# Kernel optimization log

Hardware: AMD Instinct MI355X
Metric: run time of the kernel (lower is better)

The kernel has to match this reference:

```python
import jax, jax.numpy as jnp
import numpy as np

H, W = 512, 512          # config.height, config.width
PIXEL_SIZE = 1.0
A2P = 1.0 / PIXEL_SIZE   # angstrom_to_pixel
INV_AREA = 1.0 / PIXEL_SIZE ** 2
SQRT2 = 1.4142135623730951
N, F, B = 8192, 2, 8


def setup_inputs() -> dict:
    key = jax.random.key(0)
    k1, k2, k3, k4, k5 = jax.random.split(key, 5)
    centers = jax.random.uniform(k1, (N, 3), minval=64.0, maxval=448.0)
    scales = jax.random.uniform(k2, (N, F), minval=1.0, maxval=4.0)
    weights = jax.random.normal(k3, (N, F))
    bubble_weights = 0.1 * jax.random.normal(k4, (N,))
    transform_matrix = jnp.eye(4)[None] + 0.01 * jax.random.normal(k5, (B, 4, 4))
    return {
        "transform_matrix": transform_matrix,
        "centers": centers,
        "scales": scales,
        "weights": weights,
        "bubble_weights": bubble_weights,
    }


def _pixel_profile(c, s, n):
    # Exact integral of a 1D gaussian N(c, s^2) over each unit pixel [x-0.5, x+0.5].
    # c, s: (M,) -> (M, n)
    x = jnp.arange(n, dtype=c.dtype)
    lo = (x[None, :] - 0.5 - c[:, None]) / (s[:, None] * SQRT2)
    hi = (x[None, :] + 0.5 - c[:, None]) / (s[:, None] * SQRT2)
    return 0.5 * (jax.lax.erf(hi) - jax.lax.erf(lo))


def _splat_point_masses(img, cp, w):
    # Bilinear scatter-add of point masses at projected centers cp (N,2), coord0 = row.
    r, c = cp[:, 0], cp[:, 1]
    r0f, c0f = jnp.floor(r), jnp.floor(c)
    fr, fc = r - r0f, c - c0f
    r0, c0 = r0f.astype(jnp.int32), c0f.astype(jnp.int32)
    for dr, dc, ww in ((0, 0, (1 - fr) * (1 - fc)), (0, 1, (1 - fr) * fc),
                       (1, 0, fr * (1 - fc)), (1, 1, fr * fc)):
        rr = jnp.clip(r0 + dr, 0, H - 1)
        cc = jnp.clip(c0 + dc, 0, W - 1)
        img = img.at[rr, cc].add(w * ww)
    return img


def _render_one(cp, scales_px_flat, weights_flat, bubble_weights):
    # cp: (N, 2) projected centers in pixel units.
    cpe = jnp.repeat(cp, F, axis=0)                       # (N*F, 2): expand per scale
    ph = _pixel_profile(cpe[:, 0], scales_px_flat, H)     # (N*F, H)
    pw = _pixel_profile(cpe[:, 1], scales_px_flat, W)     # (N*F, W)
    img = jnp.einsum("mh,mw->hw", weights_flat[:, None] * ph, pw)
    img = _splat_point_masses(img, cp, bubble_weights)
    return img


def reference(transform_matrix, centers, scales, weights, bubble_weights):
    # Homogenize centers: (N, 4)
    ch = jnp.concatenate([centers, jnp.ones_like(centers[:, :1])], axis=-1)
    # Solve T x = c for each (pose, gaussian): (B,1,4,4) \\ (1,N,4,1) -> (B,N,4)
    proj = jnp.linalg.solve(transform_matrix[:, None], ch[None, :, :, None])[..., 0]
    cp = proj[..., :2] / proj[..., 3:4] * A2P             # (B, N, 2) pixel coords
    scales_px = (scales * A2P).reshape(-1)                # (N*F,)
    weights_flat = weights.reshape(-1)                    # (N*F,)
    render = jax.vmap(lambda c: _render_one(c, scales_px, weights_flat, bubble_weights))
    result = render(cp) * INV_AREA                        # (B, H, W)
    return result
```

## Files before the change

### kernel.cpp

```cpp
#include <hip/hip_runtime.h>
#include <hip/hip_bf16.h>

#define HH 512
#define WW 512
#define NN 8192
#define FF 2
#define BB 8
#define MM (NN * FF)
#define HW (HH * WW)
#define NC (BB * NN)

#define NSIG 3.8f

__device__ __forceinline__ float ld(const void* p, int i, int f32mode) {
  if (f32mode) return ((const float*)p)[i];
  unsigned u = ((const unsigned short*)p)[i];
  return __uint_as_float(u << 16);
}

__device__ __forceinline__ float readlane_f(float v, int l) {
  return __uint_as_float(__builtin_amdgcn_readlane(__float_as_uint(v), l));
}

__device__ __forceinline__ float erf_f(float x) {
  float ax = fabsf(x);
  float t = 1.0f / (1.0f + 0.3275911f * ax);
  float y = t * (0.254829592f +
           t * (-0.284496736f +
           t * (1.421413741f +
           t * (-1.453152027f +
           t * 1.061405429f))));
  y = 1.0f - y * __expf(-ax * ax);
  return copysignf(y, x);
}

__global__ void k_inv(const void* __restrict__ T, float* __restrict__ invT,
                      int* __restrict__ flag) {
  int b = threadIdx.x;
  if (b >= BB) return;
  const float* Tf = (const float*)T;
  int f32mode = (fabsf(Tf[0] - 1.f) < 0.4f &&
                 fabsf(Tf[5] - 1.f) < 0.4f &&
                 fabsf(Tf[10] - 1.f) < 0.4f) ? 1 : 0;
  if (b == 0) *flag = f32mode;

  float a[4][8];
  for (int r = 0; r < 4; ++r)
    for (int c = 0; c < 4; ++c) {
      a[r][c] = ld(T, b * 16 + r * 4 + c, f32mode);
      a[r][4 + c] = (r == c) ? 1.0f : 0.0f;
    }
  for (int k = 0; k < 4; ++k) {
    int p = k; float best = fabsf(a[k][k]);
    for (int i = k + 1; i < 4; ++i) {
      float v = fabsf(a[i][k]);
      if (v > best) { best = v; p = i; }
    }
    if (p != k)
      for (int c = 0; c < 8; ++c) { float tmp = a[k][c]; a[k][c] = a[p][c]; a[p][c] = tmp; }
    float inv = 1.0f / a[k][k];
    for (int c = 0; c < 8; ++c) a[k][c] *= inv;
    for (int i = 0; i < 4; ++i) {
      if (i == k) continue;
      float f = a[i][k];
      for (int c = 0; c < 8; ++c) a[i][c] -= f * a[k][c];
    }
  }
  for (int r = 0; r < 4; ++r)
    for (int c = 0; c < 4; ++c)
      invT[b * 16 + r * 4 + c] = a[r][4 + c];
}

__global__ void k_table(const void* __restrict__ centers, const void* __restrict__ scales,
                        const void* __restrict__ weights, const void* __restrict__ bubble,
                        const float* __restrict__ invT, const int* __restrict__ flag,
                        float4* __restrict__ tabA, float4* __restrict__ tabB,
                        float4* __restrict__ img4) {
  int idx = blockIdx.x * blockDim.x + threadIdx.x;
  int stride = gridDim.x * blockDim.x;
  for (int j = idx; j < BB * HW / 4; j += stride)
    img4[j] = make_float4(0.f, 0.f, 0.f, 0.f);
  if (idx >= NC) return;
  int f32mode = *flag;
  int b = idx >> 13;
  int n = idx & (NN - 1);
  const float* Tb = invT + b * 16;
  float cx = ld(centers, 3 * n, f32mode);
  float cy = ld(centers, 3 * n + 1, f32mode);
  float cz = ld(centers, 3 * n + 2, f32mode);
  float p0 = Tb[0]  * cx + Tb[1]  * cy + Tb[2]  * cz + Tb[3];
  float p1 = Tb[4]  * cx + Tb[5]  * cy + Tb[6]  * cz + Tb[7];
  float p3 = Tb[12] * cx + Tb[13] * cy + Tb[14] * cz + Tb[15];
  float inv = 1.0f / p3;
  float4 A, Bv;
  A.x = p0 * inv;
  A.y = p1 * inv;
  A.z = ld(scales, 2 * n, f32mode);
  A.w = ld(weights, 2 * n, f32mode);
  Bv.x = ld(scales, 2 * n + 1, f32mode);
  Bv.y = ld(weights, 2 * n + 1, f32mode);
  Bv.z = ld(bubble, n, f32mode);
  Bv.w = 0.f;
  tabA[idx] = A;
  tabB[idx] = Bv;
}

__global__ void k_splat(const float4* __restrict__ tabA, const float4* __restrict__ tabB,
                        float* __restrict__ img) {
  int gid = blockIdx.x * blockDim.x + threadIdx.x;
  int lane = gid & 63;
  int nwaves = (gridDim.x * blockDim.x) >> 6;
  int wave = __builtin_amdgcn_readfirstlane(gid >> 6);

  int i = wave;
  float4 A = make_float4(0.f, 0.f, 1.f, 0.f);
  float4 Bv = make_float4(1.f, 0.f, 0.f, 0.f);
  if (i < NC) { A = tabA[i]; Bv = tabB[i]; }

  while (i < NC) {
    int in = i + nwaves;
    float4 An = A, Bn = Bv;
    if (in < NC) { An = tabA[in]; Bn = tabB[in]; }

    float row = A.x, col = A.y, s0 = A.z, w0 = A.w;
    float s1 = Bv.x, w1 = Bv.y, bw = Bv.z;
    float* imgb = img + ((size_t)(i >> 13) << 18);

    {
      float r0f = floorf(row), c0f = floorf(col);
      float fr = row - r0f, fc = col - c0f;
      int r0 = (int)r0f, c0 = (int)c0f;
      int rr0 = min(max(r0, 0), HH - 1), rr1 = min(max(r0 + 1, 0), HH - 1);
      int cc0 = min(max(c0, 0), WW - 1), cc1 = min(max(c0 + 1, 0), WW - 1);
      int rsel = (lane < 2) ? rr0 : rr1;
      int csel = (lane & 1) ? cc1 : cc0;
      float wr = (lane < 2) ? (1.f - fr) : fr;
      float wc = (lane & 1) ? fc : (1.f - fc);
      if (lane < 4)
        unsafeAtomicAdd(imgb + (rsel << 9) + csel, bw * wr * wc);
    }

    float smax = fmaxf(s0, s1);
    float rs0 = 0.70710678118f / s0;
    float rs1 = 0.70710678118f / s1;
    float Rf = NSIG * smax + 0.5f;
    int rlo = max(0, (int)ceilf(row - Rf));
    int rhi = min(HH - 1, (int)floorf(row + Rf));
    int clo = max(0, (int)ceilf(col - Rf));
    int chi = min(WW - 1, (int)floorf(col + Rf));
    if (rlo <= rhi && clo <= chi) {
      int nc = chi - clo + 1;
      int nr = rhi - rlo + 1;
      float xc = (float)(clo + lane) - 0.5f - col;
      float x0 = xc * rs0;
      float pw0 = (erf_f(x0 + rs0) - erf_f(x0)) * (0.25f * w0);
      float x1 = xc * rs1;
      float pw1 = (erf_f(x1 + rs1) - erf_f(x1)) * (0.25f * w1);
      float yr = (float)(rlo + lane) - 0.5f - row;
      float y0 = yr * rs0;
      float Dh0 = erf_f(y0 + rs0) - erf_f(y0);
      float y1 = yr * rs1;
      float Dh1 = erf_f(y1 + rs1) - erf_f(y1);
      float* base = imgb + (rlo << 9) + clo + lane;
      for (int k = 0; k < nr; ++k) {
        float val = readlane_f(Dh0, k) * pw0 + readlane_f(Dh1, k) * pw1;
        if (lane < nc)
          unsafeAtomicAdd(base + (k << 9), val);
      }
    }

    i = in; A = An; Bv = Bn;
  }
}

__global__ void k_final(const float4* __restrict__ img4, const int* __restrict__ flag,
                        void* __restrict__ out) {
  int idx = blockIdx.x * blockDim.x + threadIdx.x;
  int stride = gridDim.x * blockDim.x;
  int f32mode = *flag;
  if (f32mode) {
    float4* o = (float4*)out;
    for (int j = idx; j < BB * HW / 4; j += stride)
      o[j] = img4[j];
  } else {
    ushort4* o = (ushort4*)out;
    for (int j = idx; j < BB * HW / 4; j += stride) {
      float4 v = img4[j];
      __hip_bfloat16 h0 = __float2bfloat16(v.x);
      __hip_bfloat16 h1 = __float2bfloat16(v.y);
      __hip_bfloat16 h2 = __float2bfloat16(v.z);
      __hip_bfloat16 h3 = __float2bfloat16(v.w);
      ushort4 t;
      t.x = *reinterpret_cast<unsigned short*>(&h0);
      t.y = *reinterpret_cast<unsigned short*>(&h1);
      t.z = *reinterpret_cast<unsigned short*>(&h2);
      t.w = *reinterpret_cast<unsigned short*>(&h3);
      o[j] = t;
    }
  }
}

extern "C" void kernel_launch(void* const* d_in, const int* in_sizes, int n_in,
                              void* d_out, int out_size, void* d_ws, size_t ws_size,
                              hipStream_t stream) {
  const void* T       = d_in[0];
  const void* centers = d_in[1];
  const void* scales  = d_in[2];
  const void* weights = d_in[3];
  const void* bubble  = d_in[4];

  char* ws = (char*)d_ws;
  size_t off = 0;
  float*  img  = (float*)(ws + off);  off += (size_t)BB * HW * 4;
  float4* tabA = (float4*)(ws + off); off += (size_t)NC * 16;
  float4* tabB = (float4*)(ws + off); off += (size_t)NC * 16;
  float*  invT = (float*)(ws + off);  off += (size_t)BB * 16 * 4;
  int*    flag = (int*)(ws + off);

  k_inv<<<1, 64, 0, stream>>>(T, invT, flag);
  k_table<<<512, 256, 0, stream>>>(centers, scales, weights, bubble, invT, flag,
                                   tabA, tabB, (float4*)img);
  k_splat<<<2048, 256, 0, stream>>>(tabA, tabB, img);
  k_final<<<512, 256, 0, stream>>>((const float4*)img, flag, d_out);
}
```

Measured before the change: 540.9 us.

## Bin gaussians by image and row band before splatting for atomic locality

Adds a counting-sort pass (per-block bin counts, a scan, and a scatter fill) that reorders the per-gaussian table by image index and 64-row band. The splat kernel then reads the image index from the table instead of deriving it from position. The intent is to make concurrently running waves hit nearby image regions, improving cache locality of the atomic adds. This costs two extra small launches, a serial scan, and possibly more atomic contention on shared addresses.

```diff
diff --git a/kernel.cpp b/kernel.cpp
--- a/kernel.cpp
+++ b/kernel.cpp
@@ -11,6 +11,9 @@
 #define NC (BB * NN)
 
 #define NSIG 3.8f
+
+#define NBINS 64
+#define CBLK 256
 
 __device__ __forceinline__ float ld(const void* p, int i, int f32mode) {
   if (f32mode) return ((const float*)p)[i];
@@ -34,6 +37,26 @@
   return copysignf(y, x);
 }
 
+__device__ __forceinline__ void project(const void* centers, const float* invT,
+                                        int b, int n, int f32mode,
+                                        float& row, float& col) {
+  const float* Tb = invT + b * 16;
+  float cx = ld(centers, 3 * n, f32mode);
+  float cy = ld(centers, 3 * n + 1, f32mode);
+  float cz = ld(centers, 3 * n + 2, f32mode);
+  float p0 = Tb[0]  * cx + Tb[1]  * cy + Tb[2]  * cz + Tb[3];
+  float p1 = Tb[4]  * cx + Tb[5]  * cy + Tb[6]  * cz + Tb[7];
+  float p3 = Tb[12] * cx + Tb[13] * cy + Tb[14] * cz + Tb[15];
+  float inv = 1.0f / p3;
+  row = p0 * inv;
+  col = p1 * inv;
+}
+
+__device__ __forceinline__ int bin_of(float row, int b) {
+  int band = min(max((int)row, 0), HH - 1) >> 6;
+  return (b << 3) | band;
+}
+
 __global__ void k_inv(const void* __restrict__ T, float* __restrict__ invT,
                       int* __restrict__ flag) {
   int b = threadIdx.x;
@@ -71,38 +94,72 @@
       invT[b * 16 + r * 4 + c] = a[r][4 + c];
 }
 
-__global__ void k_table(const void* __restrict__ centers, const void* __restrict__ scales,
-                        const void* __restrict__ weights, const void* __restrict__ bubble,
-                        const float* __restrict__ invT, const int* __restrict__ flag,
-                        float4* __restrict__ tabA, float4* __restrict__ tabB,
-                        float4* __restrict__ img4) {
-  int idx = blockIdx.x * blockDim.x + threadIdx.x;
-  int stride = gridDim.x * blockDim.x;
-  for (int j = idx; j < BB * HW / 4; j += stride)
+__global__ void __launch_bounds__(CBLK)
+k_cnt(const void* __restrict__ centers, const float* __restrict__ invT,
+      const int* __restrict__ flag, int* __restrict__ blkcnt,
+      float4* __restrict__ img4) {
+  __shared__ int cnt[NBINS];
+  int tid = threadIdx.x;
+  if (tid < NBINS) cnt[tid] = 0;
+  __syncthreads();
+  int idx = blockIdx.x * CBLK + tid;
+  for (int j = idx; j < BB * HW / 4; j += NC)
     img4[j] = make_float4(0.f, 0.f, 0.f, 0.f);
-  if (idx >= NC) return;
   int f32mode = *flag;
-  int b = idx >> 13;
-  int n = idx & (NN - 1);
-  const float* Tb = invT + b * 16;
-  float cx = ld(centers, 3 * n, f32mode);
-  float cy = ld(centers, 3 * n + 1, f32mode);
-  float cz = ld(centers, 3 * n + 2, f32mode);
-  float p0 = Tb[0]  * cx + Tb[1]  * cy + Tb[2]  * cz + Tb[3];
-  float p1 = Tb[4]  * cx + Tb[5]  * cy + Tb[6]  * cz + Tb[7];
-  float p3 = Tb[12] * cx + Tb[13] * cy + Tb[14] * cz + Tb[15];
-  float inv = 1.0f / p3;
+  int b = idx >> 13, n = idx & (NN - 1);
+  float row, col;
+  project(centers, invT, b, n, f32mode, row, col);
+  atomicAdd(&cnt[bin_of(row, b)], 1);
+  __syncthreads();
+  if (tid < NBINS) blkcnt[blockIdx.x * NBINS + tid] = cnt[tid];
+}
+
+__global__ void k_scan(int* __restrict__ blkcnt) {
+  __shared__ int tot[NBINS];
+  __shared__ int base[NBINS];
+  int t = threadIdx.x;
+  int acc = 0;
+  for (int j = 0; j < CBLK; ++j) {
+    int c = blkcnt[j * NBINS + t];
+    blkcnt[j * NBINS + t] = acc;
+    acc += c;
+  }
+  tot[t] = acc;
+  __syncthreads();
+  if (t == 0) {
+    int s = 0;
+    for (int k = 0; k < NBINS; ++k) { base[k] = s; s += tot[k]; }
+  }
+  __syncthreads();
+  for (int j = 0; j < CBLK; ++j) blkcnt[j * NBINS + t] += base[t];
+}
+
+__global__ void __launch_bounds__(CBLK)
+k_fill(const void* __restrict__ centers, const void* __restrict__ scales,
+       const void* __restrict__ weights, const void* __restrict__ bubble,
+       const float* __restrict__ invT, const int* __restrict__ flag,
+       const int* __restrict__ blkbase,
+       float4* __restrict__ tabA, float4* __restrict__ tabB) {
+  __shared__ int cur[NBINS];
+  int tid = threadIdx.x;
+  if (tid < NBINS) cur[tid] = blkbase[blockIdx.x * NBINS + tid];
+  __syncthreads();
+  int idx = blockIdx.x * CBLK + tid;
+  int f32mode = *flag;
+  int b = idx >> 13, n = idx & (NN - 1);
+  float row, col;
+  project(centers, invT, b, n, f32mode, row, col);
   float4 A, Bv;
-  A.x = p0 * inv;
-  A.y = p1 * inv;
+  A.x = row; A.y = col;
   A.z = ld(scales, 2 * n, f32mode);
   A.w = ld(weights, 2 * n, f32mode);
   Bv.x = ld(scales, 2 * n + 1, f32mode);
   Bv.y = ld(weights, 2 * n + 1, f32mode);
   Bv.z = ld(bubble, n, f32mode);
-  Bv.w = 0.f;
-  tabA[idx] = A;
-  tabB[idx] = Bv;
+  Bv.w = (float)b;
+  int pos = atomicAdd(&cur[bin_of(row, b)], 1);
+  tabA[pos] = A;
+  tabB[pos] = Bv;
 }
 
 __global__ void k_splat(const float4* __restrict__ tabA, const float4* __restrict__ tabB,
@@ -124,7 +181,7 @@
 
     float row = A.x, col = A.y, s0 = A.z, w0 = A.w;
     float s1 = Bv.x, w1 = Bv.y, bw = Bv.z;
-    float* imgb = img + ((size_t)(i >> 13) << 18);
+    float* imgb = img + ((size_t)(int)Bv.w << 18);
 
     {
       float r0f = floorf(row), c0f = floorf(col);
@@ -211,15 +268,18 @@
 
   char* ws = (char*)d_ws;
   size_t off = 0;
-  float*  img  = (float*)(ws + off);  off += (size_t)BB * HW * 4;
-  float4* tabA = (float4*)(ws + off); off += (size_t)NC * 16;
-  float4* tabB = (float4*)(ws + off); off += (size_t)NC * 16;
-  float*  invT = (float*)(ws + off);  off += (size_t)BB * 16 * 4;
-  int*    flag = (int*)(ws + off);
-
-  k_inv<<<1, 64, 0, stream>>>(T, invT, flag);
-  k_table<<<512, 256, 0, stream>>>(centers, scales, weights, bubble, invT, flag,
-                                   tabA, tabB, (float4*)img);
+  float*  img   = (float*)(ws + off);  off += (size_t)BB * HW * 4;
+  float4* tabA  = (float4*)(ws + off); off += (size_t)NC * 16;
+  float4* tabB  = (float4*)(ws + off); off += (size_t)NC * 16;
+  int*    blkcnt= (int*)(ws + off);    off += (size_t)CBLK * NBINS * 4;
+  float*  invT  = (float*)(ws + off);  off += (size_t)BB * 16 * 4;
+  int*    flag  = (int*)(ws + off);
+
+  k_inv  <<<1,    64,  0, stream>>>(T, invT, flag);
+  k_cnt  <<<CBLK, CBLK, 0, stream>>>(centers, invT, flag, blkcnt, (float4*)img);
+  k_scan <<<1,    NBINS, 0, stream>>>(blkcnt);
+  k_fill <<<CBLK, CBLK, 0, stream>>>(centers, scales, weights, bubble, invT, flag,
+                                     blkcnt, tabA, tabB);
   k_splat<<<2048, 256, 0, stream>>>(tabA, tabB, img);
-  k_final<<<512, 256, 0, stream>>>((const float4*)img, flag, d_out);
-}
+  k_final<<<512,  256, 0, stream>>>((const float4*)img, flag, d_out);
+}
```

Result: slower. 568.6 us (+5.1%).
